# Kernel optimization log

Hardware: AMD Instinct MI355X
Metric: run time of the kernel (lower is better)

The kernel has to match this reference:

```python
import jax, jax.numpy as jnp
import numpy as np

N_SIGMA = 1
K_MAX = 8          # max number of non-zero instance ids
FG_W = 1.0         # foreground_weight
W_INST, W_VAR, W_SEED = 1.0, 10.0, 1.0


def _lovasz_hinge_flat(logits, labels_f):
    # logits, labels_f: [P] flat; standard Lovasz hinge (descending-error sort)
    signs = 2.0 * labels_f - 1.0
    errors = 1.0 - logits * signs
    perm = jnp.argsort(-errors)
    errors_sorted = errors[perm]
    gt_sorted = labels_f[perm]
    gts = gt_sorted.sum()
    cum = jnp.cumsum(gt_sorted)
    intersection = gts - cum
    union = gts + jnp.cumsum(1.0 - gt_sorted)
    jaccard = 1.0 - intersection / union
    grad = jnp.concatenate([jaccard[:1], jaccard[1:] - jaccard[:-1]])
    return jnp.sum(jax.nn.relu(errors_sorted) * jax.lax.stop_gradient(grad))


def _spatial_emb_loss(prediction, instances, labels):
    B, C, H, W = prediction.shape
    inst = instances[:, 0]  # [B,H,W]
    # coordinate buffer: linspace over the full 1024x2048 grid, then sliced
    xm = jnp.linspace(0.0, 2.0, 2048)[:W]
    ym = jnp.linspace(0.0, 1.0, 1024)[:H]
    xym = jnp.stack([jnp.broadcast_to(xm[None, :], (H, W)),
                     jnp.broadcast_to(ym[:, None], (H, W))])  # [2,H,W]
    ids = jnp.arange(1, K_MAX + 1)

    def per_image(pred, ins, lab):
        spatial_emb = jnp.tanh(pred[0:2]) + xym            # [2,H,W]
        sigma = pred[2]                                     # [H,W] (n_sigma=1)
        seed = jax.nn.sigmoid(pred[3])                      # [H,W]
        bg = (lab == 0)
        seed_loss_bg = jnp.sum(jnp.where(bg, seed ** 2, 0.0))
        masks = (ins[None] == ids[:, None, None])           # [K,H,W]
        mf = masks.astype(pred.dtype)
        counts = mf.sum((1, 2))                             # [K]
        present = counts > 0
        cnt = jnp.maximum(counts, 1.0)
        # to_center=True: center = mean of xym over instance pixels
        center = jnp.einsum('chw,khw->kc', xym, mf) / cnt[:, None]   # [K,2]
        s_mean = jnp.einsum('hw,khw->k', sigma, mf) / cnt            # [K]
        var_k = jnp.einsum('khw,khw->k',
                           (sigma[None] - jax.lax.stop_gradient(s_mean)[:, None, None]) ** 2,
                           mf) / cnt
        s_exp = jnp.exp(10.0 * s_mean)                                # [K]
        d2 = jnp.sum((spatial_emb[None] - center[:, :, None, None]) ** 2, axis=1)  # [K,H,W]
        dist = jnp.exp(-s_exp[:, None, None] * d2)                    # [K,H,W]
        lov = jax.vmap(_lovasz_hinge_flat)(2.0 * dist.reshape(K_MAX, -1) - 1.0,
                                           mf.reshape(K_MAX, -1))     # [K]
        seed_fg = jnp.einsum('khw,khw->k',
                             (seed[None] - jax.lax.stop_gradient(dist)) ** 2, mf)
        objf = jnp.maximum(present.sum().astype(pred.dtype), 1.0)
        inst_loss = jnp.where(present, lov, 0.0).sum() / objf
        var_loss = jnp.where(present, var_k, 0.0).sum() / objf
        seed_loss = (seed_loss_bg + FG_W * jnp.where(present, seed_fg, 0.0).sum()) / (H * W)
        return W_INST * inst_loss + W_VAR * var_loss + W_SEED * seed_loss

    per = jax.vmap(per_image)(prediction, inst, labels)
    return per.mean() + 0.0 * prediction.sum()


def setup_inputs() -> dict:
    key = jax.random.key(0)
    k1, k2, k3 = jax.random.split(key, 3)
    B, H, W = 4, 512, 1024
    prediction = jax.random.normal(k1, (B, 2 + N_SIGMA + 1, H, W), dtype=jnp.float32)
    instances = jax.random.randint(k2, (B, 1, H, W), 0, K_MAX + 1, dtype=jnp.int32)
    labels = jax.random.randint(k3, (B, H, W), 0, 2, dtype=jnp.int32)
    return {"prediction": prediction, "instances": instances, "labels": labels}


def reference(prediction, instances, labels):
    return _spatial_emb_loss(prediction, instances, labels)
```

## Files before the change

kernel.cpp:

```cpp
#include <hip/hip_runtime.h>
#include <math.h>

namespace {
constexpr int B_ = 4, K_ = 8, W_ = 1024;
constexpr int N_ = 512 * 1024;
constexpr int M_ = 128;
constexpr int MP_ = M_ + 1;
constexpr int BK_ = B_ * K_;
constexpr int KM_ = K_ * M_;

constexpr int HB_ = 1024;
constexpr int HBPB_ = HB_ / B_;
constexpr int HCH_ = N_ / HBPB_;
constexpr int SB_ = 1024;
constexpr int SBPB_ = SB_ / B_;
constexpr int SCH_ = N_ / SBPB_;
constexpr int NSTAT = 41;
constexpr int NHC_ = 4;

constexpr size_t PART_BYTES = (size_t)HB_ * KM_ * 4;
constexpr size_t SFG_OFF_B  = PART_BYTES;
constexpr size_t PSTAT_OFF_B = SFG_OFF_B + (size_t)BK_ * HBPB_ * 4;
constexpr size_t WSF_OFF_B  = PSTAT_OFF_B + (size_t)B_ * NSTAT * SBPB_ * 4;

constexpr int CNT_OFF  = 0;
constexpr int OBJF_OFF = 32;
}

__device__ __forceinline__ float fsigmoid_(float x) { return 1.0f / (1.0f + __expf(-x)); }
__device__ __forceinline__ float ftanh_(float x) { return 1.0f - 2.0f / (__expf(2.0f * x) + 1.0f); }

__global__ __launch_bounds__(256) void stats_kernel(const float* __restrict__ pred,
                                                    const int* __restrict__ inst,
                                                    const int* __restrict__ lab,
                                                    float* __restrict__ pstat,
                                                    float* __restrict__ out) {
    int tid = threadIdx.x;
    if (blockIdx.x == 0 && tid == 0) out[0] = 0.0f;
    int b = blockIdx.x >> 8;
    int blk = blockIdx.x & (SBPB_ - 1);
    int pix0 = blk * SCH_;

    const float* sigp = pred + ((long long)b * 4 + 2) * N_;
    const float* p3p  = pred + ((long long)b * 4 + 3) * N_;
    const int*   insp = inst + (long long)b * N_;
    const int*   labp = lab  + (long long)b * N_;

    float acc[NSTAT];
#pragma unroll
    for (int i = 0; i < NSTAT; i++) acc[i] = 0.0f;

#pragma unroll
    for (int it = 0; it < SCH_ / (256 * 4); it++) {
        int base = pix0 + (it * 256 + tid) * 4;
        float4 sg = *(const float4*)(sigp + base);
        float4 q3 = *(const float4*)(p3p + base);
        int4 in4 = *(const int4*)(insp + base);
        int4 lb4 = *(const int4*)(labp + base);
        float ss[4] = {sg.x, sg.y, sg.z, sg.w};
        float qq[4] = {q3.x, q3.y, q3.z, q3.w};
        int ii[4] = {in4.x, in4.y, in4.z, in4.w};
        int ll[4] = {lb4.x, lb4.y, lb4.z, lb4.w};
#pragma unroll
        for (int j = 0; j < 4; j++) {
            int pix = base + j;
            float xm = (float)(pix & (W_ - 1)) * (2.0f / 2047.0f);
            float ym = (float)(pix >> 10) * (1.0f / 1023.0f);
            float seed = fsigmoid_(qq[j]);
            if (ll[j] == 0) acc[40] += seed * seed;
            float s = ss[j];
#pragma unroll
            for (int k = 0; k < K_; k++) {
                float m = (ii[j] == k + 1) ? 1.0f : 0.0f;
                acc[k * 5]     += m;
                acc[k * 5 + 1] += m * xm;
                acc[k * 5 + 2] += m * ym;
                acc[k * 5 + 3] += m * s;
                acc[k * 5 + 4] += m * s * s;
            }
        }
    }
#pragma unroll
    for (int i = 0; i < NSTAT; i++) {
        float v = acc[i];
#pragma unroll
        for (int off = 32; off; off >>= 1) v += __shfl_down(v, off, 64);
        acc[i] = v;
    }
    __shared__ float xw[4][NSTAT];
    if ((tid & 63) == 0) {
        int w = tid >> 6;
#pragma unroll
        for (int i = 0; i < NSTAT; i++) xw[w][i] = acc[i];
    }
    __syncthreads();
    if (tid < NSTAT)
        pstat[((b * NSTAT + tid) << 8) + blk] =
            xw[0][tid] + xw[1][tid] + xw[2][tid] + xw[3][tid];
}

__global__ __launch_bounds__(256) void hist_kernel(const float* __restrict__ pred,
                                                   const int* __restrict__ inst,
                                                   const float* __restrict__ pstat,
                                                   float* __restrict__ wsf,
                                                   unsigned int* __restrict__ partial,
                                                   float* __restrict__ sfgpart,
                                                   float* __restrict__ out) {
    __shared__ float sq[NSTAT][4];
    __shared__ float ssum[NSTAT];
    __shared__ float prm[K_][4];
    __shared__ float svar[K_];
    __shared__ int spres[K_];
    __shared__ unsigned int hsh[NHC_][K_ * MP_];
    __shared__ float xfg[4][K_];

    int tid = threadIdx.x;
    int b = blockIdx.x >> 8;
    int blk = blockIdx.x & (HBPB_ - 1);
    int pix0 = blk * HCH_;

    if (tid < NSTAT * 4) {
        int row = tid >> 2, q = tid & 3;
        const float4* p = (const float4*)(pstat + ((size_t)(b * NSTAT + row) << 8)) + q * 16;
        float4 a = {0, 0, 0, 0};
#pragma unroll
        for (int j = 0; j < 16; j++) {
            float4 v = p[j];
            a.x += v.x; a.y += v.y; a.z += v.z; a.w += v.w;
        }
        sq[row][q] = (a.x + a.y) + (a.z + a.w);
    }
    for (int i = tid; i < NHC_ * K_ * MP_; i += 256) (&hsh[0][0])[i] = 0u;
    __syncthreads();
    if (tid < NSTAT) ssum[tid] = (sq[tid][0] + sq[tid][1]) + (sq[tid][2] + sq[tid][3]);
    __syncthreads();
    if (tid < K_) {
        float counts = ssum[tid * 5];
        float cnt = fmaxf(counts, 1.0f);
        float smean = ssum[tid * 5 + 3] / cnt;
        prm[tid][0] = ssum[tid * 5 + 1] / cnt;
        prm[tid][1] = ssum[tid * 5 + 2] / cnt;
        prm[tid][2] = expf(10.0f * smean);
        prm[tid][3] = counts;
        if (blk == 0) {
            svar[tid] = (counts > 0.0f) ? ssum[tid * 5 + 4] / cnt - smean * smean : 0.0f;
            spres[tid] = counts > 0.0f ? 1 : 0;
            wsf[CNT_OFF + b * K_ + tid] = counts;
        }
    }
    __syncthreads();
    if (blk == 0 && tid == 0) {
        float np = 0.0f, vl = 0.0f;
#pragma unroll
        for (int k = 0; k < K_; k++) { np += (float)spres[k]; vl += svar[k]; }
        float objf = fmaxf(np, 1.0f);
        wsf[OBJF_OFF + b] = objf;
        atomicAdd(out, (10.0f * vl / objf + ssum[40] / (float)N_) * (1.0f / (float)B_));
    }

    float cx[K_], cy[K_], sxp[K_];
    bool prs[K_];
#pragma unroll
    for (int k = 0; k < K_; k++) {
        cx[k] = prm[k][0]; cy[k] = prm[k][1]; sxp[k] = prm[k][2];
        prs[k] = prm[k][3] > 0.0f;
    }
    unsigned int* hpriv = &hsh[tid & 3][0];

    const float* p0p = pred + ((long long)b * 4) * N_;
    const float* p1p = p0p + N_;
    const float* p3p = p0p + 3LL * N_;
    const int* insp = inst + (long long)b * N_;

    float sfg[K_];
#pragma unroll
    for (int k = 0; k < K_; k++) sfg[k] = 0.0f;

#pragma unroll
    for (int it = 0; it < HCH_ / (256 * 4); it++) {
        int base = pix0 + (it * 256 + tid) * 4;
        float4 a0 = *(const float4*)(p0p + base);
        float4 a1 = *(const float4*)(p1p + base);
        float4 a3 = *(const float4*)(p3p + base);
        int4 in4 = *(const int4*)(insp + base);
        float v0[4] = {a0.x, a0.y, a0.z, a0.w};
        float v1[4] = {a1.x, a1.y, a1.z, a1.w};
        float v3[4] = {a3.x, a3.y, a3.z, a3.w};
        int ii[4] = {in4.x, in4.y, in4.z, in4.w};
#pragma unroll
        for (int j = 0; j < 4; j++) {
            int pix = base + j;
            float sex = ftanh_(v0[j]) + (float)(pix & (W_ - 1)) * (2.0f / 2047.0f);
            float sey = ftanh_(v1[j]) + (float)(pix >> 10) * (1.0f / 1023.0f);
            float seed = fsigmoid_(v3[j]);
            int ins = ii[j];
#pragma unroll
            for (int k = 0; k < K_; k++) {
                if (prs[k]) {
                    float dx = sex - cx[k];
                    float dy = sey - cy[k];
                    float dist = __expf(-sxp[k] * (dx * dx + dy * dy));
                    bool fg = (ins == k + 1);
                    int ib = (int)fminf(128.0f * dist, 127.0f);
                    int bin = fg ? 127 - ib : ib;
                    atomicAdd(hpriv + (k * MP_ + bin), fg ? 0x10001u : 1u);
                    if (fg) { float d = seed - dist; sfg[k] += d * d; }
                }
            }
        }
    }
    __syncthreads();

    unsigned int* gp = partial + (size_t)blockIdx.x * KM_;
    for (int i = tid; i < KM_; i += 256) {
        int r = (i >> 7) * MP_ + (i & (M_ - 1));
        gp[i] = hsh[0][r] + hsh[1][r] + hsh[2][r] + hsh[3][r];
    }

#pragma unroll
    for (int k = 0; k < K_; k++) {
        float v = sfg[k];
#pragma unroll
        for (int off = 32; off; off >>= 1) v += __shfl_down(v, off, 64);
        sfg[k] = v;
    }
    if ((tid & 63) == 0) {
        int w = tid >> 6;
#pragma unroll
        for (int k = 0; k < K_; k++) xfg[w][k] = sfg[k];
    }
    __syncthreads();
    if (tid < K_)
        sfgpart[(size_t)(b * K_ + tid) * HBPB_ + blk] =
            xfg[0][tid] + xfg[1][tid] + xfg[2][tid] + xfg[3][tid];
}

__global__ __launch_bounds__(1024) void lovasz_kernel(const unsigned int* __restrict__ partial,
                                                      const float* __restrict__ sfgpart,
                                                      const float* __restrict__ wsf,
                                                      float* __restrict__ out) {
    int bk = blockIdx.x;
    int b = bk >> 3, k = bk & 7;
    int tid = threadIdx.x;
    int bin = tid & (M_ - 1), grp = tid >> 7;
    constexpr int PER = HBPB_ / 8;

    const unsigned int* p = partial +
        (size_t)(b * HBPB_ + grp * PER) * KM_ + k * M_ + bin;
    unsigned int n = 0, f = 0;
#pragma unroll 8
    for (int j = 0; j < PER; j++) {
        unsigned int v = p[(size_t)j * KM_];
        n += v & 0xffffu;
        f += v >> 16;
    }

    __shared__ unsigned int gn[8][M_], gf[8][M_];
    __shared__ float lovp;
    __shared__ float xs[4];
    gn[grp][bin] = n; gf[grp][bin] = f;
    __syncthreads();

    float pcnt = wsf[CNT_OFF + bk];
    float pp = fmaxf(pcnt, 1.0f);

    if (tid < 64) {
        unsigned long long p0 = 0ull, p1 = 0ull;
#pragma unroll
        for (int g = 0; g < 8; g++) {
            uint2 vn = *(const uint2*)&gn[g][2 * tid];
            uint2 vf = *(const uint2*)&gf[g][2 * tid];
            p0 += ((unsigned long long)vn.x << 32) | (unsigned long long)vf.x;
            p1 += ((unsigned long long)vn.y << 32) | (unsigned long long)vf.y;
        }
        unsigned long long T = p0 + p1;
#pragma unroll
        for (int off = 1; off < 64; off <<= 1) {
            unsigned long long t = __shfl_down(T, off, 64);
            if (tid + off < 64) T += t;
        }
        unsigned long long S0 = T;
        unsigned long long S1 = T - p0;
        float acc;
        {
            unsigned int R = (unsigned int)(S0 >> 32), F = (unsigned int)S0;
            float J = (R == 0) ? 0.0f : (1.0f - (pp - (float)F) / (pp + (float)(R - F)));
            acc = (tid == 0 ? 0.5f : 1.0f) * J;
        }
        {
            unsigned int R = (unsigned int)(S1 >> 32), F = (unsigned int)S1;
            float J = (R == 0) ? 0.0f : (1.0f - (pp - (float)F) / (pp + (float)(R - F)));
            acc += J;
        }
#pragma unroll
        for (int off = 32; off; off >>= 1) acc += __shfl_down(acc, off, 64);
        if (tid == 0) lovp = acc;
    } else if (tid >= 256 && tid < 512) {
        float sv = sfgpart[(size_t)bk * HBPB_ + (tid - 256)];
#pragma unroll
        for (int off = 32; off; off >>= 1) sv += __shfl_down(sv, off, 64);
        if ((tid & 63) == 0) xs[(tid - 256) >> 6] = sv;
    }
    __syncthreads();

    if (tid == 0 && pcnt > 0.0f) {
        float lov = lovp * (2.0f / (float)M_);
        float sfgt = (xs[0] + xs[1]) + (xs[2] + xs[3]);
        float objf = wsf[OBJF_OFF + b];
        atomicAdd(out, (lov / objf + sfgt / (float)N_) * (1.0f / (float)B_));
    }
}

extern "C" void kernel_launch(void* const* d_in, const int* in_sizes, int n_in,
                              void* d_out, int out_size, void* d_ws, size_t ws_size,
                              hipStream_t stream) {
    const float* pred = (const float*)d_in[0];
    const int* inst = (const int*)d_in[1];
    const int* lab = (const int*)d_in[2];
    float* out = (float*)d_out;

    unsigned int* partial = (unsigned int*)d_ws;
    float* sfgpart = (float*)((char*)d_ws + SFG_OFF_B);
    float* pstat = (float*)((char*)d_ws + PSTAT_OFF_B);
    float* wsf = (float*)((char*)d_ws + WSF_OFF_B);

    stats_kernel<<<SB_, 256, 0, stream>>>(pred, inst, lab, pstat, out);
    hist_kernel<<<HB_, 256, 0, stream>>>(pred, inst, pstat, wsf, partial, sfgpart, out);
    lovasz_kernel<<<BK_, 1024, 0, stream>>>(partial, sfgpart, wsf, out);
}
```

Before: 116.8 us.

## Hoist stats finalization into a separate kernel and skip far-background histogram atomics

Moves the per-image reduction of partial statistics (centers, sigma exponent, variance and seed-background terms) out of every histogram block into a small four-block finalize kernel, which writes the parameters to workspace. This removes reduction work that each of the 1024 histogram blocks used to repeat. The histogram loop also counts background pixels whose exponent argument exceeds 5 (these always fall in bin 0) in registers, then adds them with one wave-reduced atomic instead of one shared atomic per pixel. The cost is an extra kernel launch and a branch in the inner loop. The shortcut only pays off when many pixels lie far from the instance centers.

```diff
diff --git a/kernel.cpp b/kernel.cpp
--- a/kernel.cpp
+++ b/kernel.cpp
@@ -25,6 +25,7 @@
 
 constexpr int CNT_OFF  = 0;
 constexpr int OBJF_OFF = 32;
+constexpr int PRM_OFF  = 64;
 }
 
 __device__ __forceinline__ float fsigmoid_(float x) { return 1.0f / (1.0f + __expf(-x)); }
@@ -99,18 +100,59 @@
             xw[0][tid] + xw[1][tid] + xw[2][tid] + xw[3][tid];
 }
 
+__global__ __launch_bounds__(256) void finalize_kernel(const float* __restrict__ pstat,
+                                                       float* __restrict__ wsf,
+                                                       float* __restrict__ out) {
+    __shared__ float sq[NSTAT][4];
+    __shared__ float ssum[NSTAT];
+    __shared__ float svar[K_];
+    __shared__ int spres[K_];
+    int tid = threadIdx.x;
+    int b = blockIdx.x;
+
+    if (tid < NSTAT * 4) {
+        int row = tid >> 2, q = tid & 3;
+        const float4* p = (const float4*)(pstat + ((size_t)(b * NSTAT + row) << 8)) + q * 16;
+        float4 a = {0, 0, 0, 0};
+#pragma unroll
+        for (int j = 0; j < 16; j++) {
+            float4 v = p[j];
+            a.x += v.x; a.y += v.y; a.z += v.z; a.w += v.w;
+        }
+        sq[row][q] = (a.x + a.y) + (a.z + a.w);
+    }
+    __syncthreads();
+    if (tid < NSTAT) ssum[tid] = (sq[tid][0] + sq[tid][1]) + (sq[tid][2] + sq[tid][3]);
+    __syncthreads();
+    if (tid < K_) {
+        float counts = ssum[tid * 5];
+        float cnt = fmaxf(counts, 1.0f);
+        float smean = ssum[tid * 5 + 3] / cnt;
+        wsf[PRM_OFF + (b * 3 + 0) * K_ + tid] = ssum[tid * 5 + 1] / cnt;
+        wsf[PRM_OFF + (b * 3 + 1) * K_ + tid] = ssum[tid * 5 + 2] / cnt;
+        wsf[PRM_OFF + (b * 3 + 2) * K_ + tid] = expf(10.0f * smean);
+        wsf[CNT_OFF + b * K_ + tid] = counts;
+        svar[tid] = (counts > 0.0f) ? ssum[tid * 5 + 4] / cnt - smean * smean : 0.0f;
+        spres[tid] = counts > 0.0f ? 1 : 0;
+    }
+    __syncthreads();
+    if (tid == 0) {
+        float np = 0.0f, vl = 0.0f;
+#pragma unroll
+        for (int k = 0; k < K_; k++) { np += (float)spres[k]; vl += svar[k]; }
+        float objf = fmaxf(np, 1.0f);
+        wsf[OBJF_OFF + b] = objf;
+        atomicAdd(out, (10.0f * vl / objf + ssum[40] / (float)N_) * (1.0f / (float)B_));
+    }
+}
+
 __global__ __launch_bounds__(256) void hist_kernel(const float* __restrict__ pred,
                                                    const int* __restrict__ inst,
-                                                   const float* __restrict__ pstat,
-                                                   float* __restrict__ wsf,
+                                                   const float* __restrict__ wsf,
                                                    unsigned int* __restrict__ partial,
                                                    float* __restrict__ sfgpart,
                                                    float* __restrict__ out) {
-    __shared__ float sq[NSTAT][4];
-    __shared__ float ssum[NSTAT];
-    __shared__ float prm[K_][4];
-    __shared__ float svar[K_];
-    __shared__ int spres[K_];
+    __shared__ float prm[4][K_];
     __shared__ unsigned int hsh[NHC_][K_ * MP_];
     __shared__ float xfg[4][K_];
 
@@ -119,51 +161,21 @@
     int blk = blockIdx.x & (HBPB_ - 1);
     int pix0 = blk * HCH_;
 
-    if (tid < NSTAT * 4) {
-        int row = tid >> 2, q = tid & 3;
-        const float4* p = (const float4*)(pstat + ((size_t)(b * NSTAT + row) << 8)) + q * 16;
-        float4 a = {0, 0, 0, 0};
-#pragma unroll
-        for (int j = 0; j < 16; j++) {
-            float4 v = p[j];
-            a.x += v.x; a.y += v.y; a.z += v.z; a.w += v.w;
-        }
-        sq[row][q] = (a.x + a.y) + (a.z + a.w);
+    if (tid < K_) {
+        prm[0][tid] = wsf[PRM_OFF + (b * 3 + 0) * K_ + tid];
+        prm[1][tid] = wsf[PRM_OFF + (b * 3 + 1) * K_ + tid];
+        prm[2][tid] = wsf[PRM_OFF + (b * 3 + 2) * K_ + tid];
+        prm[3][tid] = wsf[CNT_OFF + b * K_ + tid];
     }
     for (int i = tid; i < NHC_ * K_ * MP_; i += 256) (&hsh[0][0])[i] = 0u;
     __syncthreads();
-    if (tid < NSTAT) ssum[tid] = (sq[tid][0] + sq[tid][1]) + (sq[tid][2] + sq[tid][3]);
-    __syncthreads();
-    if (tid < K_) {
-        float counts = ssum[tid * 5];
-        float cnt = fmaxf(counts, 1.0f);
-        float smean = ssum[tid * 5 + 3] / cnt;
-        prm[tid][0] = ssum[tid * 5 + 1] / cnt;
-        prm[tid][1] = ssum[tid * 5 + 2] / cnt;
-        prm[tid][2] = expf(10.0f * smean);
-        prm[tid][3] = counts;
-        if (blk == 0) {
-            svar[tid] = (counts > 0.0f) ? ssum[tid * 5 + 4] / cnt - smean * smean : 0.0f;
-            spres[tid] = counts > 0.0f ? 1 : 0;
-            wsf[CNT_OFF + b * K_ + tid] = counts;
-        }
-    }
-    __syncthreads();
-    if (blk == 0 && tid == 0) {
-        float np = 0.0f, vl = 0.0f;
-#pragma unroll
-        for (int k = 0; k < K_; k++) { np += (float)spres[k]; vl += svar[k]; }
-        float objf = fmaxf(np, 1.0f);
-        wsf[OBJF_OFF + b] = objf;
-        atomicAdd(out, (10.0f * vl / objf + ssum[40] / (float)N_) * (1.0f / (float)B_));
-    }
 
     float cx[K_], cy[K_], sxp[K_];
     bool prs[K_];
 #pragma unroll
     for (int k = 0; k < K_; k++) {
-        cx[k] = prm[k][0]; cy[k] = prm[k][1]; sxp[k] = prm[k][2];
-        prs[k] = prm[k][3] > 0.0f;
+        cx[k] = prm[0][k]; cy[k] = prm[1][k]; sxp[k] = prm[2][k];
+        prs[k] = prm[3][k] > 0.0f;
     }
     unsigned int* hpriv = &hsh[tid & 3][0];
 
@@ -173,8 +185,9 @@
     const int* insp = inst + (long long)b * N_;
 
     float sfg[K_];
-#pragma unroll
-    for (int k = 0; k < K_; k++) sfg[k] = 0.0f;
+    unsigned int n0[K_];
+#pragma unroll
+    for (int k = 0; k < K_; k++) { sfg[k] = 0.0f; n0[k] = 0u; }
 
 #pragma unroll
     for (int it = 0; it < HCH_ / (256 * 4); it++) {
@@ -199,15 +212,27 @@
                 if (prs[k]) {
                     float dx = sex - cx[k];
                     float dy = sey - cy[k];
-                    float dist = __expf(-sxp[k] * (dx * dx + dy * dy));
+                    float t = sxp[k] * (dx * dx + dy * dy);
                     bool fg = (ins == k + 1);
-                    int ib = (int)fminf(128.0f * dist, 127.0f);
-                    int bin = fg ? 127 - ib : ib;
-                    atomicAdd(hpriv + (k * MP_ + bin), fg ? 0x10001u : 1u);
-                    if (fg) { float d = seed - dist; sfg[k] += d * d; }
+                    if (!fg && t > 5.0f) {
+                        n0[k]++;
+                    } else {
+                        float dist = __expf(-t);
+                        int ib = (int)fminf(128.0f * dist, 127.0f);
+                        int bin = fg ? 127 - ib : ib;
+                        atomicAdd(hpriv + (k * MP_ + bin), fg ? 0x10001u : 1u);
+                        if (fg) { float d = seed - dist; sfg[k] += d * d; }
+                    }
                 }
             }
         }
+    }
+#pragma unroll
+    for (int k = 0; k < K_; k++) {
+        unsigned int v = n0[k];
+#pragma unroll
+        for (int off = 32; off; off >>= 1) v += __shfl_down(v, off, 64);
+        if ((tid & 63) == 0 && v) atomicAdd(hpriv + k * MP_, v);
     }
     __syncthreads();
 
@@ -325,6 +350,7 @@
     float* wsf = (float*)((char*)d_ws + WSF_OFF_B);
 
     stats_kernel<<<SB_, 256, 0, stream>>>(pred, inst, lab, pstat, out);
-    hist_kernel<<<HB_, 256, 0, stream>>>(pred, inst, pstat, wsf, partial, sfgpart, out);
+    finalize_kernel<<<B_, 256, 0, stream>>>(pstat, wsf, out);
+    hist_kernel<<<HB_, 256, 0, stream>>>(pred, inst, wsf, partial, sfgpart, out);
     lovasz_kernel<<<BK_, 1024, 0, stream>>>(partial, sfgpart, wsf, out);
 }
```

New measurement: 123.1 us. +5.4%, slower.
